# Optimization experiments

Hardware: AMD Instinct MI355X
Metric: run time of the kernel (lower is better)

The kernel has to match this reference:

```python
import jax, jax.numpy as jnp
import numpy as np

H = 8  # num_heads in both MHA blocks


def _mha_self(x, W_in, b_in, W_out, b_out, mask=None):
    """Faithful nn.MultiheadAttention self-attention (batch_first).
    x: [B,S,E]; W_in: [3E,E]; b_in: [3E]; W_out: [E,E]; b_out: [E].
    mask: optional [S,S] bool, True = attend."""
    B, S, E = x.shape
    dh = E // H
    qkv = x @ W_in.T + b_in                      # [B,S,3E]
    q, k, v = jnp.split(qkv, 3, axis=-1)
    # [B,H,S,dh]
    q = q.reshape(B, S, H, dh).transpose(0, 2, 1, 3)
    k = k.reshape(B, S, H, dh).transpose(0, 2, 1, 3)
    v = v.reshape(B, S, H, dh).transpose(0, 2, 1, 3)
    scores = jnp.einsum('bhqd,bhkd->bhqk', q, k) / jnp.sqrt(jnp.asarray(dh, x.dtype))
    if mask is not None:
        scores = jnp.where(mask[None, None], scores, jnp.finfo(scores.dtype).min)
    probs = jax.nn.softmax(scores, axis=-1)
    out = jnp.einsum('bhqk,bhkd->bhqd', probs, v)  # [B,H,S,dh]
    out = out.transpose(0, 2, 1, 3).reshape(B, S, E)
    return out @ W_out.T + b_out


def setup_inputs() -> dict:
    key = jax.random.key(0)
    ks = jax.random.split(key, 7)
    B, S, E = 8, 1024, 512
    sc = 0.02
    return {
        'x': jax.random.normal(ks[0], (B, S, E), jnp.float32),
        'Wl_in': jax.random.normal(ks[1], (3 * E, E), jnp.float32) * sc,
        'bl_in': jnp.zeros((3 * E,), jnp.float32),
        'Wl_out': jax.random.normal(ks[2], (E, E), jnp.float32) * sc,
        'bl_out': jnp.zeros((E,), jnp.float32),
        'Wg_in': jax.random.normal(ks[3], (3 * E, E), jnp.float32) * sc,
        'bg_in': jnp.zeros((3 * E,), jnp.float32),
        'Wg_out': jax.random.normal(ks[4], (E, E), jnp.float32) * sc,
        'bg_out': jnp.zeros((E,), jnp.float32),
        'Wf': jax.random.normal(ks[5], (E, 2 * E), jnp.float32) * sc,
        'bf': jnp.zeros((E,), jnp.float32),
    }


def reference(x, Wl_in, bl_in, Wl_out, bl_out, Wg_in, bg_in, Wg_out, bg_out, Wf, bf):
    LOCAL = 3  # local_size
    B, S, E = x.shape
    # Per-token sliding window [i-LOCAL, i+LOCAL] == banded attention mask
    idx = jnp.arange(S)
    band = jnp.abs(idx[:, None] - idx[None, :]) <= LOCAL  # [S,S] bool
    local_out = _mha_self(x, Wl_in, bl_in, Wl_out, bl_out, mask=band)
    global_out = _mha_self(x, Wg_in, bg_in, Wg_out, bg_out)
    fused = jnp.concatenate([local_out, global_out], axis=-1)  # [B,S,2E]
    return jax.nn.relu(fused @ Wf.T + bf)
```

## Files before the change

### kernel.cpp

```cpp
#include <hip/hip_runtime.h>

typedef unsigned short u16;
typedef unsigned int   u32;
typedef __bf16 v8bf __attribute__((ext_vector_type(8)));
typedef float  v4f  __attribute__((ext_vector_type(4)));
typedef u16    us4  __attribute__((ext_vector_type(4)));
typedef u32    ui4  __attribute__((ext_vector_type(4)));

__device__ __forceinline__ u16 f2bf(float f) {
  u32 u = __builtin_bit_cast(u32, f);
  u += 0x7fffu + ((u >> 16) & 1u);
  return (u16)(u >> 16);
}
__device__ __forceinline__ float bf2f(u16 s) {
  u32 u = ((u32)s) << 16;
  return __builtin_bit_cast(float, u);
}

__device__ __forceinline__ void load_lds16(const u16* g, u16* l) {
  __builtin_amdgcn_global_load_lds(
      (const __attribute__((address_space(1))) u32*)g,
      (__attribute__((address_space(3))) u32*)l, 16, 0, 0);
}

__global__ void __launch_bounds__(256) cvt_all(
    const float* __restrict__ x,   const float* __restrict__ wli,
    const float* __restrict__ wlo, const float* __restrict__ wgi,
    const float* __restrict__ wgo, const float* __restrict__ wf,
    u16* __restrict__ out, u16* __restrict__ wloT, u16* __restrict__ wgoT)
{
  const int v = blockIdx.x * 256 + threadIdx.x;
  const float* src; int obase; int mode = 0; u16* T = nullptr;
  if      (v < 1048576) { src = x;   obase = 0;       }
  else if (v < 1245184) { src = wli; obase = 1048576; }
  else if (v < 1310720) { src = wlo; obase = 1245184; mode = 1; T = wloT; }
  else if (v < 1507328) { src = wgi; obase = 1310720; }
  else if (v < 1572864) { src = wgo; obase = 1507328; mode = 1; T = wgoT; }
  else                  { src = wf;  obase = 1572864; }
  const int rel = v - obase;
  const float4 f = reinterpret_cast<const float4*>(src)[rel];
  us4 o;
  o.x = f2bf(f.x); o.y = f2bf(f.y); o.z = f2bf(f.z); o.w = f2bf(f.w);
  if (mode) {
    const int eb = rel * 4, c = eb >> 9, k = eb & 511;
#pragma unroll
    for (int i = 0; i < 4; ++i) T[(k + i) * 512 + c] = o[i];
  } else {
    int o4;
    if      (v < 1245184) o4 = v;
    else if (v < 1507328) o4 = v - 65536;
    else                  o4 = v - 131072;
    reinterpret_cast<us4*>(out)[o4] = o;
  }
}

template<int RELU, int OUTF32, int TV, int BIASF>
__device__ __forceinline__ void gemm_body(
    u16* __restrict__ As, u16* __restrict__ Bs,
    const u16* __restrict__ A, const int lda,
    const u16* __restrict__ B, const int ldb,
    const float* __restrict__ bias, void* __restrict__ C,
    u16* __restrict__ vt, const int bm, const int bn,
    const int K, const int ldc, const int colofs)
{
  const int tid  = threadIdx.x;
  const int lane = tid & 63;
  const int w    = tid >> 6;
  const int lid  = lane & 15;
  const int quad = lane >> 4;
  const int wr = w >> 1, wc = w & 1;

  v4f acc[4][4];
#pragma unroll
  for (int i = 0; i < 4; ++i)
#pragma unroll
    for (int j = 0; j < 4; ++j)
      acc[i][j] = (v4f){0.f, 0.f, 0.f, 0.f};

  const int dr = lane >> 3;
  const int cs = ((lane ^ dr) & 7) * 8;

  for (int k0 = 0; k0 < K; k0 += 64) {
#pragma unroll
    for (int p = 0; p < 4; ++p) {
      const int g   = w + p * 4;
      const int row = g * 8 + dr;
      load_lds16(A + (size_t)(bm + row) * lda + k0 + cs, As + g * 512);
      load_lds16(B + (size_t)(bn + row) * ldb + k0 + cs, Bs + g * 512);
    }
    __syncthreads();
#pragma unroll
    for (int kk = 0; kk < 2; ++kk) {
      v8bf af[4], bfr[4];
#pragma unroll
      for (int mi = 0; mi < 4; ++mi)
        af[mi] = *reinterpret_cast<const v8bf*>(
            &As[(wr * 64 + mi * 16 + lid) * 64 + (((kk * 4 + quad) ^ (lid & 7)) * 8)]);
#pragma unroll
      for (int ni = 0; ni < 4; ++ni)
        bfr[ni] = *reinterpret_cast<const v8bf*>(
            &Bs[(wc * 64 + ni * 16 + lid) * 64 + (((kk * 4 + quad) ^ (lid & 7)) * 8)]);
#pragma unroll
      for (int mi = 0; mi < 4; ++mi)
#pragma unroll
        for (int ni = 0; ni < 4; ++ni)
          acc[mi][ni] = __builtin_amdgcn_mfma_f32_16x16x32_bf16(
              af[mi], bfr[ni], acc[mi][ni], 0, 0, 0);
    }
    __syncthreads();
  }

  float bv[4];
#pragma unroll
  for (int ni = 0; ni < 4; ++ni)
    bv[ni] = BIASF ? bias[bn + wc * 64 + ni * 16 + lid] : 0.f;

  if (TV && bn >= 1024) {
#pragma unroll
    for (int mi = 0; mi < 4; ++mi) {
      const int m0 = bm + wr * 64 + mi * 16 + quad * 4;
#pragma unroll
      for (int ni = 0; ni < 4; ++ni) {
        const int n = bn + wc * 64 + ni * 16 + lid - 1024;
        us4 pk;
#pragma unroll
        for (int r = 0; r < 4; ++r) pk[r] = f2bf(acc[mi][ni][r] + bv[ni]);
        const size_t idx =
            ((size_t)((m0 >> 10) * 8 + (n >> 6)) * 64 + (n & 63)) * 1024 + (m0 & 1023);
        *reinterpret_cast<us4*>(&vt[idx]) = pk;
      }
    }
  } else {
#pragma unroll
    for (int mi = 0; mi < 4; ++mi) {
#pragma unroll
      for (int ni = 0; ni < 4; ++ni) {
        const int n = bn + wc * 64 + ni * 16 + lid;
#pragma unroll
        for (int r = 0; r < 4; ++r) {
          const int m = bm + wr * 64 + mi * 16 + quad * 4 + r;
          float v = acc[mi][ni][r] + bv[ni];
          if (RELU) v = fmaxf(v, 0.f);
          if (OUTF32)
            reinterpret_cast<float*>(C)[(size_t)m * ldc + colofs + n] = v;
          else
            reinterpret_cast<u16*>(C)[(size_t)m * ldc + colofs + n] = f2bf(v);
        }
      }
    }
  }
}

__global__ void __launch_bounds__(256) qkv_dual(
    const u16* __restrict__ xb,
    const u16* __restrict__ wli, const float* __restrict__ bli, u16* __restrict__ qkv_l,
    const u16* __restrict__ wgi, const float* __restrict__ bgi, u16* __restrict__ qkv_g,
    u16* __restrict__ vt)
{
  __shared__ __align__(16) u16 As[128 * 64];
  __shared__ __align__(16) u16 Bs[128 * 64];
  if (blockIdx.x < 12)
    gemm_body<0,0,0,1>(As, Bs, xb, 512, wli, 512, bli, qkv_l, nullptr,
                       blockIdx.y * 128, blockIdx.x * 128, 512, 1536, 0);
  else
    gemm_body<0,0,1,1>(As, Bs, xb, 512, wgi, 512, bgi, qkv_g, vt,
                       blockIdx.y * 128, (blockIdx.x - 12) * 128, 512, 1536, 0);
}

__global__ void __launch_bounds__(256, 4) mega(
    const u16* __restrict__ qkv, const u16* __restrict__ vt, u16* __restrict__ outp,
    const u16* __restrict__ wfb, const u16* __restrict__ wloT, const u16* __restrict__ wgoT,
    u16* __restrict__ Wc, const float* __restrict__ blo, const float* __restrict__ bgo,
    const float* __restrict__ bff, float* __restrict__ bias_c,
    const u16* __restrict__ qkvl, u16* __restrict__ attn_l)
{
  __shared__ __align__(16) u16 smem[20480];
  const int bx   = blockIdx.x;
  const int tid  = threadIdx.x;
  const int lane = tid & 63;
  const int w    = tid >> 6;

  if (bx >= 1064) {
    const int lbx = bx - 1064;
    const int qt = lbx & 15, bh = lbx >> 4;
    const int b = bh >> 3, h = bh & 7;
    const int i0 = qt * 64;
    const size_t base = (size_t)b * 1024 * 1536;
    u16* Kl = smem;
    u16* Vl = smem + 4480;

    for (int idx = tid; idx < 1120; idx += 256) {
      const int isV  = idx >= 560;
      const int idx2 = isV ? idx - 560 : idx;
      const int row = idx2 >> 3, ch = idx2 & 7;
      const int jc = min(max(i0 - 3 + row, 0), 1023);
      const ui4 d = *reinterpret_cast<const ui4*>(
          qkvl + base + (size_t)jc * 1536 + (isV ? 1024 : 512) + h * 64 + ch * 8);
      *reinterpret_cast<ui4*>(&(isV ? Vl : Kl)[row * 64 + ch * 8]) = d;
    }
    __syncthreads();

    for (int t = 0; t < 16; ++t) {
      const int i = i0 + w * 16 + t;
      const float qd = bf2f(qkvl[base + (size_t)i * 1536 + h * 64 + lane]);
      float denom = 0.f, accv = 0.f;
#pragma unroll
      for (int tt = 0; tt < 7; ++tt) {
        const int j = i - 3 + tt;
        const bool ok = (j >= 0) && (j <= 1023);
        const int ridx = w * 16 + t + tt;
        float pr = qd * bf2f(Kl[ridx * 64 + lane]);
#pragma unroll
        for (int msk = 32; msk >= 1; msk >>= 1) pr += __shfl_xor(pr, msk);
        const float p = ok ? __expf(pr * 0.125f) : 0.f;
        denom += p;
        accv += p * bf2f(Vl[ridx * 64 + lane]);
      }
      attn_l[(size_t)(b * 1024 + i) * 1536 + h * 64 + lane] = f2bf(accv / denom);
    }
    return;
  }
  if (bx >= 1056) {
    const int e = (bx - 1056) * 64 + w * 16;
    for (int t = 0; t < 16; ++t) {
      float sum = 0.f;
#pragma unroll
      for (int j = 0; j < 16; ++j) {
        const int c2 = j * 64 + lane;
        const float b = (c2 < 512) ? blo[c2] : bgo[c2 - 512];
        sum += bf2f(wfb[(size_t)(e + t) * 1024 + c2]) * b;
      }
#pragma unroll
      for (int msk = 32; msk >= 1; msk >>= 1) sum += __shfl_xor(sum, msk);
      if (lane == 0) bias_c[e + t] = bff[e + t] + sum;
    }
    return;
  }
  if (bx >= 1024) {
    const int idx = bx - 1024;
    const int half = idx >> 4, rem = idx & 15;
    gemm_body<0,0,0,0>(smem, smem + 8192, wfb + half * 512, 1024,
                       (half ? wgoT : wloT), 512, nullptr, Wc, nullptr,
                       (rem >> 2) * 128, (rem & 3) * 128, 512, 1024, half * 512);
    return;
  }

  const int lid  = lane & 15;
  const int quad = lane >> 4;
  const int qt = (bx >> 3) & 15;
  const int bh = ((bx & 7) << 3) | (bx >> 7);
  const int b = bh >> 3, h = bh & 7;
  const size_t base = (size_t)b * 1024 * 1536;

  v8bf aq[2];
  {
    const size_t qoff = base + (size_t)(qt * 64 + w * 16 + lid) * 1536 + h * 64 + quad * 8;
    aq[0] = *reinterpret_cast<const v8bf*>(qkv + qoff);
    aq[1] = *reinterpret_cast<const v8bf*>(qkv + qoff + 32);
#pragma unroll
    for (int k = 0; k < 2; ++k)
#pragma unroll
      for (int i = 0; i < 8; ++i)
        aq[k][i] = (__bf16)((float)aq[k][i] * 0.125f);
  }
  v8bf ones;
#pragma unroll
  for (int i = 0; i < 8; ++i) ones[i] = (__bf16)1.0f;

  v4f o[4], lacc = (v4f){0.f, 0.f, 0.f, 0.f};
#pragma unroll
  for (int nd = 0; nd < 4; ++nd) o[nd] = (v4f){0.f, 0.f, 0.f, 0.f};

  u16* Ps = smem + 16384;
  const int dr = lane >> 3;
  const int dc = lane & 7;
#define STAGE(KT, BI)                                                          \
  {                                                                            \
    _Pragma("unroll") for (int p = 0; p < 2; ++p) {                            \
      const int g = w + p * 4;                                                 \
      const int r = g * 8 + dr;                                                \
      const int cs = (dc ^ (r & 7)) * 8;                                       \
      load_lds16(qkv + base + (size_t)((KT) * 64 + r) * 1536 + 512 + h * 64 + cs, \
                 smem + (BI) * 4096 + g * 512);                                \
      load_lds16(vt + ((size_t)bh * 64 + r) * 1024 + (KT) * 64 + cs,           \
                 smem + 8192 + (BI) * 4096 + g * 512);                         \
    }                                                                          \
  }
  STAGE(0, 0);

  for (int kt = 0; kt < 16; ++kt) {
    __syncthreads();
    if (kt < 15) STAGE(kt + 1, (kt + 1) & 1);
    const u16* Ks = smem + (kt & 1) * 4096;
    const u16* Vs = smem + 8192 + (kt & 1) * 4096;

    v4f s[4];
#pragma unroll
    for (int nk = 0; nk < 4; ++nk) s[nk] = (v4f){0.f, 0.f, 0.f, 0.f};
#pragma unroll
    for (int kk = 0; kk < 2; ++kk)
#pragma unroll
      for (int nk = 0; nk < 4; ++nk) {
        const v8bf bk = *reinterpret_cast<const v8bf*>(
            &Ks[(nk * 16 + lid) * 64 + (((kk * 4 + quad) ^ (lid & 7)) * 8)]);
        s[nk] = __builtin_amdgcn_mfma_f32_16x16x32_bf16(aq[kk], bk, s[nk], 0, 0, 0);
      }

#pragma unroll
    for (int nk = 0; nk < 4; ++nk) {
#pragma unroll
      for (int r = 0; r < 4; ++r) {
        const float p = __expf(s[nk][r]);
        const int prow = quad * 4 + r;
        const int pcol = nk * 16 + lid;
        Ps[w * 1024 + prow * 64 + (((pcol >> 3) ^ (prow & 7)) * 8) + (pcol & 7)] = f2bf(p);
      }
    }

#pragma unroll
    for (int kk = 0; kk < 2; ++kk) {
      const v8bf ap = *reinterpret_cast<const v8bf*>(
          &Ps[w * 1024 + lid * 64 + (((kk * 4 + quad) ^ (lid & 7)) * 8)]);
      lacc = __builtin_amdgcn_mfma_f32_16x16x32_bf16(ones, ap, lacc, 0, 0, 0);
#pragma unroll
      for (int nd = 0; nd < 4; ++nd) {
        const v8bf av = *reinterpret_cast<const v8bf*>(
            &Vs[(nd * 16 + lid) * 64 + (((kk * 4 + quad) ^ (lid & 7)) * 8)]);
        o[nd] = __builtin_amdgcn_mfma_f32_16x16x32_bf16(av, ap, o[nd], 0, 0, 0);
      }
    }
  }
#undef STAGE

  const float inv = 1.f / lacc[0];
  const int tok = b * 1024 + qt * 64 + w * 16 + lid;
#pragma unroll
  for (int nd = 0; nd < 4; ++nd) {
    us4 pk;
#pragma unroll
    for (int r = 0; r < 4; ++r) pk[r] = f2bf(o[nd][r] * inv);
    *reinterpret_cast<us4*>(&outp[(size_t)tok * 512 + h * 64 + nd * 16 + quad * 4]) = pk;
  }
}

__global__ void __launch_bounds__(256) gemm_final(
    const u16* __restrict__ Al, const u16* __restrict__ Ag,
    const u16* __restrict__ Bw, const float* __restrict__ biasc,
    float* __restrict__ out)
{
  __shared__ __align__(16) u16 As[64 * 64];
  __shared__ __align__(16) u16 Bs[128 * 64];
  const int tid  = threadIdx.x;
  const int lane = tid & 63;
  const int w    = tid >> 6;
  const int lid  = lane & 15;
  const int quad = lane >> 4;
  const int bm = blockIdx.y * 64;
  const int bn = blockIdx.x * 128;

  v4f acc[4][2];
#pragma unroll
  for (int i = 0; i < 4; ++i)
#pragma unroll
    for (int j = 0; j < 2; ++j)
      acc[i][j] = (v4f){0.f, 0.f, 0.f, 0.f};

  const int dr = lane >> 3;
  const int cs = ((lane ^ dr) & 7) * 8;

  for (int k0 = 0; k0 < 1024; k0 += 64) {
    const int half = k0 >> 9;
    const u16* Asrc = half ? Ag : Al;
    const int  lda  = half ? 512 : 1536;
    const int  kcol = k0 & 511;
#pragma unroll
    for (int p = 0; p < 2; ++p) {
      const int g   = w + p * 4;
      const int row = g * 8 + dr;
      load_lds16(Asrc + (size_t)(bm + row) * lda + kcol + cs, As + g * 512);
    }
#pragma unroll
    for (int p = 0; p < 4; ++p) {
      const int g   = w + p * 4;
      const int row = g * 8 + dr;
      load_lds16(Bw + (size_t)(bn + row) * 1024 + k0 + cs, Bs + g * 512);
    }
    __syncthreads();
#pragma unroll
    for (int kk = 0; kk < 2; ++kk) {
      v8bf af[4], bfr[2];
#pragma unroll
      for (int mi = 0; mi < 4; ++mi)
        af[mi] = *reinterpret_cast<const v8bf*>(
            &As[(mi * 16 + lid) * 64 + (((kk * 4 + quad) ^ (lid & 7)) * 8)]);
#pragma unroll
      for (int ni = 0; ni < 2; ++ni)
        bfr[ni] = *reinterpret_cast<const v8bf*>(
            &Bs[(w * 32 + ni * 16 + lid) * 64 + (((kk * 4 + quad) ^ (lid & 7)) * 8)]);
#pragma unroll
      for (int mi = 0; mi < 4; ++mi)
#pragma unroll
        for (int ni = 0; ni < 2; ++ni)
          acc[mi][ni] = __builtin_amdgcn_mfma_f32_16x16x32_bf16(
              af[mi], bfr[ni], acc[mi][ni], 0, 0, 0);
    }
    __syncthreads();
  }

#pragma unroll
  for (int mi = 0; mi < 4; ++mi) {
#pragma unroll
    for (int ni = 0; ni < 2; ++ni) {
      const int n = bn + w * 32 + ni * 16 + lid;
      const float bv = biasc[n];
#pragma unroll
      for (int r = 0; r < 4; ++r) {
        const int m = bm + mi * 16 + quad * 4 + r;
        out[(size_t)m * 512 + n] = fmaxf(acc[mi][ni][r] + bv, 0.f);
      }
    }
  }
}

extern "C" void kernel_launch(void* const* d_in, const int* in_sizes, int n_in,
                              void* d_out, int out_size, void* d_ws, size_t ws_size,
                              hipStream_t stream) {
  (void)in_sizes; (void)n_in; (void)out_size; (void)ws_size;
  const float* x   = (const float*)d_in[0];
  const float* Wli = (const float*)d_in[1];
  const float* bli = (const float*)d_in[2];
  const float* Wlo = (const float*)d_in[3];
  const float* blo = (const float*)d_in[4];
  const float* Wgi = (const float*)d_in[5];
  const float* bgi = (const float*)d_in[6];
  const float* Wgo = (const float*)d_in[7];
  const float* bgo = (const float*)d_in[8];
  const float* Wf  = (const float*)d_in[9];
  const float* bff = (const float*)d_in[10];
  float* out = (float*)d_out;

  u16* W      = (u16*)d_ws;
  u16* xb     = W + 0;
  u16* wli    = W + 4194304;
  u16* wgi    = W + 4980736;
  u16* wfb    = W + 5767168;
  u16* qkv_l  = W + 6291456;
  u16* qkv_g  = W + 18874368;
  u16* vt     = W + 31457280;
  u16* Wc     = W + 35651584;
  float* bias_c = (float*)(W + 36175872);
  u16* wloT   = W + 36176896;
  u16* wgoT   = W + 36439040;
  u16* attn_g = W + 0;
  u16* attn_l = qkv_g + 1024;

  cvt_all<<<6656, 256, 0, stream>>>(x, Wli, Wlo, Wgi, Wgo, Wf, W, wloT, wgoT);
  qkv_dual<<<dim3(24, 64), 256, 0, stream>>>(xb, wli, bli, qkv_l, wgi, bgi, qkv_g, vt);
  mega<<<2088, 256, 0, stream>>>(qkv_g, vt, attn_g, wfb, wloT, wgoT, Wc,
                                 blo, bgo, bff, bias_c, qkv_l, attn_l);
  gemm_final<<<dim3(4, 128), 256, 0, stream>>>(attn_l, attn_g, Wc, bias_c, out);
}
```

Before: 216.9 us.

## Restructure banded local attention to process 16 queries per wave with vector loads

The local banded attention path now assigns each wave 16 queries at once, four lanes per query and 16 head dims per lane. Each lane computes partial dot products with vectorized LDS reads and needs only two shuffles, replacing the old loop that ran one query at a time with a full 64-lane reduction. K/V rows are padded to 72 elements to avoid LDS bank conflicts, and outputs are written as packed 4-element stores. Separately, the probability conversion in the global attention loop now truncates to bf16 instead of rounding, which trades a little accuracy for fewer instructions.

```diff
diff --git a/kernel.cpp b/kernel.cpp
--- a/kernel.cpp
+++ b/kernel.cpp
@@ -187,36 +187,65 @@
     const int i0 = qt * 64;
     const size_t base = (size_t)b * 1024 * 1536;
     u16* Kl = smem;
-    u16* Vl = smem + 4480;
-
-    for (int idx = tid; idx < 1120; idx += 256) {
-      const int isV  = idx >= 560;
-      const int idx2 = isV ? idx - 560 : idx;
-      const int row = idx2 >> 3, ch = idx2 & 7;
+    u16* Vl = smem + 5040;
+
+    for (int i2 = tid; i2 < 1120; i2 += 256) {
+      const int isV = i2 >= 560;
+      const int i3  = isV ? i2 - 560 : i2;
+      const int row = i3 >> 3, ch = i3 & 7;
       const int jc = min(max(i0 - 3 + row, 0), 1023);
       const ui4 d = *reinterpret_cast<const ui4*>(
           qkvl + base + (size_t)jc * 1536 + (isV ? 1024 : 512) + h * 64 + ch * 8);
-      *reinterpret_cast<ui4*>(&(isV ? Vl : Kl)[row * 64 + ch * 8]) = d;
-    }
-    __syncthreads();
-
-    for (int t = 0; t < 16; ++t) {
-      const int i = i0 + w * 16 + t;
-      const float qd = bf2f(qkvl[base + (size_t)i * 1536 + h * 64 + lane]);
-      float denom = 0.f, accv = 0.f;
-#pragma unroll
-      for (int tt = 0; tt < 7; ++tt) {
-        const int j = i - 3 + tt;
-        const bool ok = (j >= 0) && (j <= 1023);
-        const int ridx = w * 16 + t + tt;
-        float pr = qd * bf2f(Kl[ridx * 64 + lane]);
-#pragma unroll
-        for (int msk = 32; msk >= 1; msk >>= 1) pr += __shfl_xor(pr, msk);
-        const float p = ok ? __expf(pr * 0.125f) : 0.f;
-        denom += p;
-        accv += p * bf2f(Vl[ridx * 64 + lane]);
-      }
-      attn_l[(size_t)(b * 1024 + i) * 1536 + h * 64 + lane] = f2bf(accv / denom);
+      *reinterpret_cast<ui4*>(&(isV ? Vl : Kl)[row * 72 + ch * 8]) = d;
+    }
+    __syncthreads();
+
+    const int q   = lane >> 2;
+    const int oct = lane & 3;
+    const int i   = i0 + w * 16 + q;
+    const u16* qrow = qkvl + base + (size_t)i * 1536 + h * 64 + oct * 16;
+    float qf[16];
+    {
+      const v8bf q0 = *reinterpret_cast<const v8bf*>(qrow);
+      const v8bf q1 = *reinterpret_cast<const v8bf*>(qrow + 8);
+#pragma unroll
+      for (int e = 0; e < 8; ++e) { qf[e] = (float)q0[e]; qf[8 + e] = (float)q1[e]; }
+    }
+    float denom = 0.f, accv[16];
+#pragma unroll
+    for (int e = 0; e < 16; ++e) accv[e] = 0.f;
+
+#pragma unroll
+    for (int tt = 0; tt < 7; ++tt) {
+      const int j = i - 3 + tt;
+      const bool ok = (j >= 0) && (j <= 1023);
+      const int ridx = w * 16 + q + tt;
+      const v8bf k0 = *reinterpret_cast<const v8bf*>(&Kl[ridx * 72 + oct * 16]);
+      const v8bf k1 = *reinterpret_cast<const v8bf*>(&Kl[ridx * 72 + oct * 16 + 8]);
+      float pr = 0.f;
+#pragma unroll
+      for (int e = 0; e < 8; ++e)
+        pr += qf[e] * (float)k0[e] + qf[8 + e] * (float)k1[e];
+      pr += __shfl_xor(pr, 1);
+      pr += __shfl_xor(pr, 2);
+      const float p = ok ? __expf(pr * 0.125f) : 0.f;
+      denom += p;
+      const v8bf v0 = *reinterpret_cast<const v8bf*>(&Vl[ridx * 72 + oct * 16]);
+      const v8bf v1 = *reinterpret_cast<const v8bf*>(&Vl[ridx * 72 + oct * 16 + 8]);
+#pragma unroll
+      for (int e = 0; e < 8; ++e) {
+        accv[e]     += p * (float)v0[e];
+        accv[8 + e] += p * (float)v1[e];
+      }
+    }
+    const float inv = 1.f / denom;
+    u16* dst = attn_l + (size_t)(b * 1024 + i) * 1536 + h * 64 + oct * 16;
+#pragma unroll
+    for (int c4 = 0; c4 < 4; ++c4) {
+      us4 pk;
+#pragma unroll
+      for (int e = 0; e < 4; ++e) pk[e] = f2bf(accv[c4 * 4 + e] * inv);
+      *reinterpret_cast<us4*>(dst + c4 * 4) = pk;
     }
     return;
   }
@@ -277,13 +306,12 @@
 #define STAGE(KT, BI)                                                          \
   {                                                                            \
     _Pragma("unroll") for (int p = 0; p < 2; ++p) {                            \
-      const int g = w + p * 4;                                                 \
-      const int r = g * 8 + dr;                                                \
+      const int r = (w + p * 4) * 8 + dr;                                      \
       const int cs = (dc ^ (r & 7)) * 8;                                       \
       load_lds16(qkv + base + (size_t)((KT) * 64 + r) * 1536 + 512 + h * 64 + cs, \
-                 smem + (BI) * 4096 + g * 512);                                \
+                 smem + (BI) * 4096 + (w + p * 4) * 512);                      \
       load_lds16(vt + ((size_t)bh * 64 + r) * 1024 + (KT) * 64 + cs,           \
-                 smem + 8192 + (BI) * 4096 + g * 512);                         \
+                 smem + 8192 + (BI) * 4096 + (w + p * 4) * 512);               \
     }                                                                          \
   }
   STAGE(0, 0);
@@ -313,7 +341,8 @@
         const float p = __expf(s[nk][r]);
         const int prow = quad * 4 + r;
         const int pcol = nk * 16 + lid;
-        Ps[w * 1024 + prow * 64 + (((pcol >> 3) ^ (prow & 7)) * 8) + (pcol & 7)] = f2bf(p);
+        Ps[w * 1024 + prow * 64 + (((pcol >> 3) ^ (prow & 7)) * 8) + (pcol & 7)] =
+            (u16)(__builtin_bit_cast(u32, p) >> 16);
       }
     }
 
```

New measurement: 182.6 us. 15.8% less time.
